# Kernel optimization log

Measured on AMD Instinct MI355X. Metric: run time of the kernel, lower is better.

Reference implementation:

```python
import jax, jax.numpy as jnp
import numpy as np

B = 16384
MV = 512   # movie_vector_size
UV = 512   # user_vector_size
NM = 16    # num_dense_movie_embeddings
NU = 16    # num_dense_user_embeddings
DS = 16    # dense_embedding_size
MLP = [256, 128, 1]


def setup_inputs() -> dict:
    key = jax.random.key(0)
    ks = jax.random.split(key, 12)
    inp = {
        'movie_vectors': jax.random.normal(ks[0], (B, MV), jnp.float32),
        'user_vectors': jax.random.normal(ks[1], (B, UV), jnp.float32),
        # embedding towers: Linear(in, DS*N + 1), stored as [in, out]
        'Wm': jax.random.normal(ks[2], (MV, DS * NM + 1), jnp.float32) * (1.0 / np.sqrt(MV)),
        'bm': jax.random.normal(ks[3], (DS * NM + 1,), jnp.float32) * 0.01,
        'Wu': jax.random.normal(ks[4], (UV, DS * NU + 1), jnp.float32) * (1.0 / np.sqrt(UV)),
        'bu': jax.random.normal(ks[5], (DS * NU + 1,), jnp.float32) * 0.01,
    }
    d_in = (NM + NU) * DS  # 512
    dims = [d_in] + MLP
    for i in range(len(MLP)):
        inp[f'W{i+1}'] = jax.random.normal(ks[6 + 2*i], (dims[i], dims[i+1]), jnp.float32) * (1.0 / np.sqrt(dims[i]))
        inp[f'b{i+1}'] = jax.random.normal(ks[7 + 2*i], (dims[i+1],), jnp.float32) * 0.01
    return inp


def reference(movie_vectors, user_vectors, Wm, bm, Wu, bu, W1, b1, W2, b2, W3, b3):
    batch = movie_vectors.shape[0]
    movie_dense = movie_vectors @ Wm + bm          # [B, DS*NM+1]
    user_dense = user_vectors @ Wu + bu            # [B, DS*NU+1]
    fm_additive = movie_dense[:, -1] + user_dense[:, -1]            # [B]
    m_split = movie_dense[:, :-1].reshape(batch, NM, DS)            # [B, NM, DS]
    u_split = user_dense[:, :-1].reshape(batch, NU, DS)             # [B, NU, DS]
    fm_interactions = jnp.einsum('bik,bjk->bij', m_split, u_split).reshape(batch, -1)  # [B, NM*NU]
    all_dense = jnp.concatenate([movie_dense[:, :-1], user_dense[:, :-1]], axis=-1)    # [B, (NM+NU)*DS]
    h = jax.nn.relu(all_dense @ W1 + b1)
    h = jax.nn.relu(h @ W2 + b2)
    mlp_out = h @ W3 + b3                                           # [B, 1]
    logit = mlp_out + fm_additive[:, None] + jnp.sum(fm_interactions, axis=-1, keepdims=True)
    return logit
```

## Files before the change

kernel.cpp:

```cpp
#include <hip/hip_runtime.h>


#define NTH 512
#define RB  32

typedef __bf16 bf16x8 __attribute__((ext_vector_type(8)));
typedef float  f32x4  __attribute__((ext_vector_type(4)));

#define WS_WMF  0
#define WS_WUF  294912
#define WS_W1F  589824
#define WS_W2F  851968
#define WS_BIAS 917504

#define BPITCH  528
#define L_BST   0
#define L_DENSE 33792
#define L_FM    66560
#define L_ADD   70912
#define L_OUT   71168
#define LDSB    71296

__device__ __forceinline__ unsigned short f2bf(float f) {
  unsigned u = __builtin_bit_cast(unsigned, f);
  u += 0x7FFFu + ((u >> 16) & 1u);
  return (unsigned short)(u >> 16);
}

__device__ __forceinline__ f32x4 mfma_bf16(bf16x8 a, bf16x8 b, f32x4 c) {
  return __builtin_amdgcn_mfma_f32_16x16x32_bf16(a, b, c, 0, 0, 0);
}

extern "C" __global__ __launch_bounds__(256) void deepfm_prep(
    const float* __restrict__ Wm, const float* __restrict__ bm,
    const float* __restrict__ Wu, const float* __restrict__ bu,
    const float* __restrict__ W1, const float* __restrict__ W2,
    const float* __restrict__ b3, char* __restrict__ ws) {
  const int unit = blockIdx.x * 4 + (threadIdx.x >> 6);
  if (unit >= 897) return;
  const int l = threadIdx.x & 63;
  const int fi = l & 15, q = l >> 4;
  unsigned short h[8];
  if (unit < 576) {
    const int t = unit / 288, rem = unit % 288;
    const int kg = rem / 18, ft = rem % 18;
    const float* W = t ? Wu : Wm;
    char* outp = ws + (t ? WS_WUF : WS_WMF);
    const int f = ft * 16 + fi;
#pragma unroll
    for (int e = 0; e < 8; ++e) {
      const int k = kg * 32 + q * 8 + e;
      float val;
      if (f < 256) val = W[k * 257 + f];
      else if (f < 272) {
        float s = 0.f;
#pragma unroll
        for (int i = 0; i < 16; ++i) s += W[k * 257 + i * 16 + (f - 256)];
        val = s;
      } else if (f == 272) val = W[k * 257 + 256];
      else val = 0.f;
      h[e] = f2bf(val);
    }
    uint4 o;
    o.x = h[0] | ((unsigned)h[1] << 16); o.y = h[2] | ((unsigned)h[3] << 16);
    o.z = h[4] | ((unsigned)h[5] << 16); o.w = h[6] | ((unsigned)h[7] << 16);
    *(uint4*)(outp + (((kg * 18 + ft) * 64 + l) << 4)) = o;
  } else if (unit < 832) {
    const int bb = unit - 576;
    const int kg = bb / 16, ft = bb % 16;
    const int f = ft * 16 + fi;
#pragma unroll
    for (int e = 0; e < 8; ++e) h[e] = f2bf(W1[(kg * 32 + q * 8 + e) * 256 + f]);
    uint4 o;
    o.x = h[0] | ((unsigned)h[1] << 16); o.y = h[2] | ((unsigned)h[3] << 16);
    o.z = h[4] | ((unsigned)h[5] << 16); o.w = h[6] | ((unsigned)h[7] << 16);
    *(uint4*)(ws + WS_W1F + (((kg * 16 + ft) * 64 + l) << 4)) = o;
  } else if (unit < 896) {
    const int bb = unit - 832;
    const int kg = bb / 8, ft = bb % 8;
    const int f = ft * 16 + fi;
#pragma unroll
    for (int e = 0; e < 8; ++e) h[e] = f2bf(W2[(kg * 32 + q * 8 + e) * 128 + f]);
    uint4 o;
    o.x = h[0] | ((unsigned)h[1] << 16); o.y = h[2] | ((unsigned)h[3] << 16);
    o.z = h[4] | ((unsigned)h[5] << 16); o.w = h[6] | ((unsigned)h[7] << 16);
    *(uint4*)(ws + WS_W2F + (((kg * 8 + ft) * 64 + l) << 4)) = o;
  } else {
    float* aux = (float*)(ws + WS_BIAS);
    if (l < 16) {
      float s = 0.f;
      for (int i = 0; i < 16; ++i) s += bm[i * 16 + l];
      aux[l] = s;
    } else if (l < 32) {
      const int k = l - 16;
      float s = 0.f;
      for (int i = 0; i < 16; ++i) s += bu[i * 16 + k];
      aux[l] = s;
    } else if (l == 32) {
      aux[32] = bm[256] + bu[256] + b3[0];
    }
  }
}

extern "C" __global__ __launch_bounds__(NTH, 4) void deepfm_main(
    const float* __restrict__ movie, const float* __restrict__ user,
    const float* __restrict__ bm, const float* __restrict__ bu,
    const float* __restrict__ b1, const float* __restrict__ b2,
    const float* __restrict__ W3, const char* __restrict__ ws,
    float* __restrict__ out) {
  extern __shared__ __align__(16) char lds[];
  char* const bstage    = lds + L_BST;
  char* const densefrag = lds + L_DENSE;
  char* const h1frag    = lds + L_BST;
  float* const fmbuf    = (float*)(lds + L_FM);
  float* const addbuf   = (float*)(lds + L_ADD);
  float* const outpart  = (float*)(lds + L_OUT);

  const int tid = threadIdx.x;
  const int w   = tid >> 6;
  const int l   = tid & 63;
  const int cn  = l & 15;
  const int q   = l >> 4;
  const int row0 = blockIdx.x * RB;

  const int tw   = w >> 2;
  const int wi   = w & 3;
  const int axi  = wi & 1;
  const int axrt = wi >> 1;

  const f32x4 zz = {0.f, 0.f, 0.f, 0.f};
  const float* auxb = (const float*)(ws + WS_BIAS);

  {
    const char* WF = ws + (tw ? WS_WUF : WS_WMF);
    const char* brow = bstage + tw * 32 * BPITCH;
    f32x4 a0r0 = zz, a0r1 = zz, a1r0 = zz, a1r1 = zz;
    f32x4 a2r0 = zz, a2r1 = zz, a3r0 = zz, a3r1 = zz;
    f32x4 axc = zz;

    for (int h = 0; h < 2; ++h) {
      if (h) __syncthreads();
#pragma unroll
      for (int p = 0; p < 8; ++p) {
        const int idx = p * 512 + tid;
        const int r = idx >> 6, f4 = idx & 63;
        const float* src = (r >= 32) ? user : movie;
        const float4 v = *(const float4*)(src + (size_t)(row0 + (r & 31)) * 512 +
                                          h * 256 + f4 * 4);
        uint2 o;
        o.x = f2bf(v.x) | ((unsigned)f2bf(v.y) << 16);
        o.y = f2bf(v.z) | ((unsigned)f2bf(v.w) << 16);
        *(uint2*)(bstage + r * BPITCH + f4 * 8) = o;
      }
      __syncthreads();

#pragma unroll 2
      for (int kgl = 0; kgl < 8; ++kgl) {
        const int kg = h * 8 + kgl;
        const bf16x8 bf0 = *(const bf16x8*)(brow + cn * BPITCH + kgl * 64 + q * 16);
        const bf16x8 bf1 = *(const bf16x8*)(brow + (16 + cn) * BPITCH + kgl * 64 + q * 16);
        const bf16x8 A0 = *(const bf16x8*)(WF + (((kg * 18 + wi * 4 + 0) * 64 + l) << 4));
        const bf16x8 A1 = *(const bf16x8*)(WF + (((kg * 18 + wi * 4 + 1) * 64 + l) << 4));
        const bf16x8 A2 = *(const bf16x8*)(WF + (((kg * 18 + wi * 4 + 2) * 64 + l) << 4));
        const bf16x8 A3 = *(const bf16x8*)(WF + (((kg * 18 + wi * 4 + 3) * 64 + l) << 4));
        const bf16x8 AX = *(const bf16x8*)(WF + (((kg * 18 + 16 + axi) * 64 + l) << 4));
        a0r0 = mfma_bf16(A0, bf0, a0r0);  a0r1 = mfma_bf16(A0, bf1, a0r1);
        a1r0 = mfma_bf16(A1, bf0, a1r0);  a1r1 = mfma_bf16(A1, bf1, a1r1);
        a2r0 = mfma_bf16(A2, bf0, a2r0);  a2r1 = mfma_bf16(A2, bf1, a2r1);
        a3r0 = mfma_bf16(A3, bf0, a3r0);  a3r1 = mfma_bf16(A3, bf1, a3r1);
        axc  = mfma_bf16(AX, axrt ? bf1 : bf0, axc);
      }
    }

    const float* bt = tw ? bu : bm;
    const f32x4 accA[4][2] = {{a0r0, a0r1}, {a1r0, a1r1}, {a2r0, a2r1}, {a3r0, a3r1}};
#pragma unroll
    for (int s = 0; s < 4; ++s) {
      const int ft = wi * 4 + s;
      const int fb = ft * 16 + q * 4;
      const float g0 = bt[fb], g1 = bt[fb + 1], g2 = bt[fb + 2], g3 = bt[fb + 3];
      const int kd = tw * 256 + fb;
      const int kgd = kd >> 5, qd = (kd >> 3) & 3, ed = kd & 4;
#pragma unroll
      for (int rt = 0; rt < 2; ++rt) {
        const f32x4 v = accA[s][rt];
        uint2 p;
        p.x = f2bf(v[0] + g0) | ((unsigned)f2bf(v[1] + g1) << 16);
        p.y = f2bf(v[2] + g2) | ((unsigned)f2bf(v[3] + g3) << 16);
        *(uint2*)(densefrag + (((kgd * 2 + rt) * 64 + qd * 16 + cn) << 4) +
                  (ed ? 8 : 0)) = p;
      }
    }

    if (axi == 0) {
#pragma unroll
      for (int reg = 0; reg < 4; ++reg)
        fmbuf[(tw * 32 + axrt * 16 + cn) * 17 + (q * 4 + reg)] = axc[reg];
    } else if (q == 0) {
      addbuf[tw * 32 + axrt * 16 + cn] = axc[0];
    }
  }

  __syncthreads();

  if (tid < 32) {
    float p = 0.f;
#pragma unroll
    for (int k = 0; k < 16; ++k)
      p += (fmbuf[tid * 17 + k] + auxb[k]) *
           (fmbuf[(32 + tid) * 17 + k] + auxb[16 + k]);
    outpart[tid] = p + addbuf[tid] + addbuf[32 + tid] + auxb[32];
  }

  {
    const char* W1F = ws + WS_W1F;
    f32x4 a00 = zz, a01 = zz, a10 = zz, a11 = zz;
#pragma unroll 4
    for (int kg = 0; kg < 16; ++kg) {
      const bf16x8 b0  = *(const bf16x8*)(densefrag + (((kg * 2 + 0) * 64 + l) << 4));
      const bf16x8 b1f = *(const bf16x8*)(densefrag + (((kg * 2 + 1) * 64 + l) << 4));
      const bf16x8 a0 = *(const bf16x8*)(W1F + (((kg * 16 + w) * 64 + l) << 4));
      const bf16x8 a1 = *(const bf16x8*)(W1F + (((kg * 16 + w + 8) * 64 + l) << 4));
      a00 = mfma_bf16(a0, b0,  a00);
      a01 = mfma_bf16(a0, b1f, a01);
      a10 = mfma_bf16(a1, b0,  a10);
      a11 = mfma_bf16(a1, b1f, a11);
    }
    const f32x4 accA[2][2] = {{a00, a01}, {a10, a11}};
#pragma unroll
    for (int s = 0; s < 2; ++s) {
      const int ft = w + s * 8;
      const int fb = ft * 16 + q * 4;
      const float g0 = b1[fb], g1 = b1[fb + 1], g2 = b1[fb + 2], g3 = b1[fb + 3];
      const int kgd = fb >> 5, qd = (fb >> 3) & 3, ed = fb & 4;
#pragma unroll
      for (int rt = 0; rt < 2; ++rt) {
        const f32x4 v = accA[s][rt];
        uint2 p;
        p.x = f2bf(fmaxf(v[0] + g0, 0.f)) | ((unsigned)f2bf(fmaxf(v[1] + g1, 0.f)) << 16);
        p.y = f2bf(fmaxf(v[2] + g2, 0.f)) | ((unsigned)f2bf(fmaxf(v[3] + g3, 0.f)) << 16);
        *(uint2*)(h1frag + (((kgd * 2 + rt) * 64 + qd * 16 + cn) << 4) +
                  (ed ? 8 : 0)) = p;
      }
    }
  }

  __syncthreads();

  {
    const char* W2F = ws + WS_W2F;
    f32x4 d0 = zz, d1 = zz;
#pragma unroll 4
    for (int kg = 0; kg < 8; ++kg) {
      const bf16x8 b0  = *(const bf16x8*)(h1frag + (((kg * 2 + 0) * 64 + l) << 4));
      const bf16x8 b1f = *(const bf16x8*)(h1frag + (((kg * 2 + 1) * 64 + l) << 4));
      const bf16x8 a0 = *(const bf16x8*)(W2F + (((kg * 8 + w) * 64 + l) << 4));
      d0 = mfma_bf16(a0, b0,  d0);
      d1 = mfma_bf16(a0, b1f, d1);
    }
    const int fb = w * 16 + q * 4;
    float bb[4], ww[4];
#pragma unroll
    for (int i = 0; i < 4; ++i) { bb[i] = b2[fb + i]; ww[i] = W3[fb + i]; }
    const f32x4 acc3[2] = {d0, d1};
#pragma unroll
    for (int rt = 0; rt < 2; ++rt) {
      float p = 0.f;
#pragma unroll
      for (int reg = 0; reg < 4; ++reg)
        p += fmaxf(acc3[rt][reg] + bb[reg], 0.f) * ww[reg];
      p += __shfl_xor(p, 16, 64);
      p += __shfl_xor(p, 32, 64);
      if (l < 16) atomicAdd(&outpart[rt * 16 + cn], p);
    }
  }

  __syncthreads();
  if (tid < 32) out[row0 + tid] = outpart[tid];
}

extern "C" void kernel_launch(void* const* d_in, const int* in_sizes, int n_in,
                              void* d_out, int out_size, void* d_ws, size_t ws_size,
                              hipStream_t stream) {
  const float* movie = (const float*)d_in[0];
  const float* user  = (const float*)d_in[1];
  const float* Wm = (const float*)d_in[2];
  const float* bm = (const float*)d_in[3];
  const float* Wu = (const float*)d_in[4];
  const float* bu = (const float*)d_in[5];
  const float* W1 = (const float*)d_in[6];
  const float* b1 = (const float*)d_in[7];
  const float* W2 = (const float*)d_in[8];
  const float* b2 = (const float*)d_in[9];
  const float* W3 = (const float*)d_in[10];
  const float* b3 = (const float*)d_in[11];
  char* ws = (char*)d_ws;
  float* out = (float*)d_out;

  (void)hipFuncSetAttribute((const void*)deepfm_main,
                            hipFuncAttributeMaxDynamicSharedMemorySize, LDSB);

  deepfm_prep<<<225, 256, 0, stream>>>(Wm, bm, Wu, bu, W1, W2, b3, ws);
  deepfm_main<<<512, NTH, LDSB, stream>>>(movie, user, bm, bu, b1, b2, W3, ws, out);
}
```

Baseline: 136.4 us.

## Double rows per block to 64 with 1024 threads, remapping wave work

Each block now handles 64 batch rows with 16 waves instead of 32 rows with 8 waves. Waves are remapped so that each weight fragment loaded from global memory feeds four row tiles instead of two. This halves the number of global weight-fragment loads per row in the embedding tower and W1 stages, and the launch drops to 256 blocks. In exchange LDS use roughly doubles to about 142 KB per block, so at most one block fits per CU, and 256 blocks may underfill a 256-CU MI355X and limit latency hiding.

```diff
diff --git a/kernel.cpp b/kernel.cpp
--- a/kernel.cpp
+++ b/kernel.cpp
@@ -1,8 +1,8 @@
 #include <hip/hip_runtime.h>
 
 
-#define NTH 512
-#define RB  32
+#define NTH 1024
+#define RB  64
 
 typedef __bf16 bf16x8 __attribute__((ext_vector_type(8)));
 typedef float  f32x4  __attribute__((ext_vector_type(4)));
@@ -15,11 +15,11 @@
 
 #define BPITCH  528
 #define L_BST   0
-#define L_DENSE 33792
-#define L_FM    66560
-#define L_ADD   70912
-#define L_OUT   71168
-#define LDSB    71296
+#define L_DENSE 67584
+#define L_FM    133120
+#define L_ADD   141824
+#define L_OUT   142336
+#define LDSB    142592
 
 __device__ __forceinline__ unsigned short f2bf(float f) {
   unsigned u = __builtin_bit_cast(unsigned, f);
@@ -123,8 +123,8 @@
   const int q   = l >> 4;
   const int row0 = blockIdx.x * RB;
 
-  const int tw   = w >> 2;
-  const int wi   = w & 3;
+  const int tw   = w >> 3;
+  const int wi   = w & 7;
   const int axi  = wi & 1;
   const int axrt = wi >> 1;
 
@@ -133,19 +133,19 @@
 
   {
     const char* WF = ws + (tw ? WS_WUF : WS_WMF);
-    const char* brow = bstage + tw * 32 * BPITCH;
-    f32x4 a0r0 = zz, a0r1 = zz, a1r0 = zz, a1r1 = zz;
-    f32x4 a2r0 = zz, a2r1 = zz, a3r0 = zz, a3r1 = zz;
+    const char* brow = bstage + tw * 64 * BPITCH;
+    f32x4 a0r0 = zz, a0r1 = zz, a0r2 = zz, a0r3 = zz;
+    f32x4 a1r0 = zz, a1r1 = zz, a1r2 = zz, a1r3 = zz;
     f32x4 axc = zz;
 
     for (int h = 0; h < 2; ++h) {
       if (h) __syncthreads();
 #pragma unroll
       for (int p = 0; p < 8; ++p) {
-        const int idx = p * 512 + tid;
+        const int idx = p * 1024 + tid;
         const int r = idx >> 6, f4 = idx & 63;
-        const float* src = (r >= 32) ? user : movie;
-        const float4 v = *(const float4*)(src + (size_t)(row0 + (r & 31)) * 512 +
+        const float* src = (r >= 64) ? user : movie;
+        const float4 v = *(const float4*)(src + (size_t)(row0 + (r & 63)) * 512 +
                                           h * 256 + f4 * 4);
         uint2 o;
         o.x = f2bf(v.x) | ((unsigned)f2bf(v.y) << 16);
@@ -159,35 +159,37 @@
         const int kg = h * 8 + kgl;
         const bf16x8 bf0 = *(const bf16x8*)(brow + cn * BPITCH + kgl * 64 + q * 16);
         const bf16x8 bf1 = *(const bf16x8*)(brow + (16 + cn) * BPITCH + kgl * 64 + q * 16);
-        const bf16x8 A0 = *(const bf16x8*)(WF + (((kg * 18 + wi * 4 + 0) * 64 + l) << 4));
-        const bf16x8 A1 = *(const bf16x8*)(WF + (((kg * 18 + wi * 4 + 1) * 64 + l) << 4));
-        const bf16x8 A2 = *(const bf16x8*)(WF + (((kg * 18 + wi * 4 + 2) * 64 + l) << 4));
-        const bf16x8 A3 = *(const bf16x8*)(WF + (((kg * 18 + wi * 4 + 3) * 64 + l) << 4));
+        const bf16x8 bf2 = *(const bf16x8*)(brow + (32 + cn) * BPITCH + kgl * 64 + q * 16);
+        const bf16x8 bf3 = *(const bf16x8*)(brow + (48 + cn) * BPITCH + kgl * 64 + q * 16);
+        const bf16x8 A0 = *(const bf16x8*)(WF + (((kg * 18 + wi * 2 + 0) * 64 + l) << 4));
+        const bf16x8 A1 = *(const bf16x8*)(WF + (((kg * 18 + wi * 2 + 1) * 64 + l) << 4));
         const bf16x8 AX = *(const bf16x8*)(WF + (((kg * 18 + 16 + axi) * 64 + l) << 4));
         a0r0 = mfma_bf16(A0, bf0, a0r0);  a0r1 = mfma_bf16(A0, bf1, a0r1);
+        a0r2 = mfma_bf16(A0, bf2, a0r2);  a0r3 = mfma_bf16(A0, bf3, a0r3);
         a1r0 = mfma_bf16(A1, bf0, a1r0);  a1r1 = mfma_bf16(A1, bf1, a1r1);
-        a2r0 = mfma_bf16(A2, bf0, a2r0);  a2r1 = mfma_bf16(A2, bf1, a2r1);
-        a3r0 = mfma_bf16(A3, bf0, a3r0);  a3r1 = mfma_bf16(A3, bf1, a3r1);
-        axc  = mfma_bf16(AX, axrt ? bf1 : bf0, axc);
+        a1r2 = mfma_bf16(A1, bf2, a1r2);  a1r3 = mfma_bf16(A1, bf3, a1r3);
+        const bf16x8 bsel = (axrt == 0) ? bf0 : (axrt == 1) ? bf1
+                          : (axrt == 2) ? bf2 : bf3;
+        axc = mfma_bf16(AX, bsel, axc);
       }
     }
 
     const float* bt = tw ? bu : bm;
-    const f32x4 accA[4][2] = {{a0r0, a0r1}, {a1r0, a1r1}, {a2r0, a2r1}, {a3r0, a3r1}};
-#pragma unroll
-    for (int s = 0; s < 4; ++s) {
-      const int ft = wi * 4 + s;
+    const f32x4 accA[2][4] = {{a0r0, a0r1, a0r2, a0r3}, {a1r0, a1r1, a1r2, a1r3}};
+#pragma unroll
+    for (int s = 0; s < 2; ++s) {
+      const int ft = wi * 2 + s;
       const int fb = ft * 16 + q * 4;
       const float g0 = bt[fb], g1 = bt[fb + 1], g2 = bt[fb + 2], g3 = bt[fb + 3];
       const int kd = tw * 256 + fb;
       const int kgd = kd >> 5, qd = (kd >> 3) & 3, ed = kd & 4;
 #pragma unroll
-      for (int rt = 0; rt < 2; ++rt) {
+      for (int rt = 0; rt < 4; ++rt) {
         const f32x4 v = accA[s][rt];
         uint2 p;
         p.x = f2bf(v[0] + g0) | ((unsigned)f2bf(v[1] + g1) << 16);
         p.y = f2bf(v[2] + g2) | ((unsigned)f2bf(v[3] + g3) << 16);
-        *(uint2*)(densefrag + (((kgd * 2 + rt) * 64 + qd * 16 + cn) << 4) +
+        *(uint2*)(densefrag + (((kgd * 4 + rt) * 64 + qd * 16 + cn) << 4) +
                   (ed ? 8 : 0)) = p;
       }
     }
@@ -195,53 +197,50 @@
     if (axi == 0) {
 #pragma unroll
       for (int reg = 0; reg < 4; ++reg)
-        fmbuf[(tw * 32 + axrt * 16 + cn) * 17 + (q * 4 + reg)] = axc[reg];
+        fmbuf[(tw * 64 + axrt * 16 + cn) * 17 + (q * 4 + reg)] = axc[reg];
     } else if (q == 0) {
-      addbuf[tw * 32 + axrt * 16 + cn] = axc[0];
+      addbuf[tw * 64 + axrt * 16 + cn] = axc[0];
     }
   }
 
   __syncthreads();
 
-  if (tid < 32) {
+  if (tid < 64) {
     float p = 0.f;
 #pragma unroll
     for (int k = 0; k < 16; ++k)
       p += (fmbuf[tid * 17 + k] + auxb[k]) *
-           (fmbuf[(32 + tid) * 17 + k] + auxb[16 + k]);
-    outpart[tid] = p + addbuf[tid] + addbuf[32 + tid] + auxb[32];
+           (fmbuf[(64 + tid) * 17 + k] + auxb[16 + k]);
+    outpart[tid] = p + addbuf[tid] + addbuf[64 + tid] + auxb[32];
   }
 
   {
     const char* W1F = ws + WS_W1F;
-    f32x4 a00 = zz, a01 = zz, a10 = zz, a11 = zz;
+    f32x4 r0 = zz, r1 = zz, r2 = zz, r3 = zz;
 #pragma unroll 4
     for (int kg = 0; kg < 16; ++kg) {
-      const bf16x8 b0  = *(const bf16x8*)(densefrag + (((kg * 2 + 0) * 64 + l) << 4));
-      const bf16x8 b1f = *(const bf16x8*)(densefrag + (((kg * 2 + 1) * 64 + l) << 4));
+      const bf16x8 b0 = *(const bf16x8*)(densefrag + (((kg * 4 + 0) * 64 + l) << 4));
+      const bf16x8 b1f = *(const bf16x8*)(densefrag + (((kg * 4 + 1) * 64 + l) << 4));
+      const bf16x8 b2f = *(const bf16x8*)(densefrag + (((kg * 4 + 2) * 64 + l) << 4));
+      const bf16x8 b3f = *(const bf16x8*)(densefrag + (((kg * 4 + 3) * 64 + l) << 4));
       const bf16x8 a0 = *(const bf16x8*)(W1F + (((kg * 16 + w) * 64 + l) << 4));
-      const bf16x8 a1 = *(const bf16x8*)(W1F + (((kg * 16 + w + 8) * 64 + l) << 4));
-      a00 = mfma_bf16(a0, b0,  a00);
-      a01 = mfma_bf16(a0, b1f, a01);
-      a10 = mfma_bf16(a1, b0,  a10);
-      a11 = mfma_bf16(a1, b1f, a11);
-    }
-    const f32x4 accA[2][2] = {{a00, a01}, {a10, a11}};
-#pragma unroll
-    for (int s = 0; s < 2; ++s) {
-      const int ft = w + s * 8;
-      const int fb = ft * 16 + q * 4;
-      const float g0 = b1[fb], g1 = b1[fb + 1], g2 = b1[fb + 2], g3 = b1[fb + 3];
-      const int kgd = fb >> 5, qd = (fb >> 3) & 3, ed = fb & 4;
-#pragma unroll
-      for (int rt = 0; rt < 2; ++rt) {
-        const f32x4 v = accA[s][rt];
-        uint2 p;
-        p.x = f2bf(fmaxf(v[0] + g0, 0.f)) | ((unsigned)f2bf(fmaxf(v[1] + g1, 0.f)) << 16);
-        p.y = f2bf(fmaxf(v[2] + g2, 0.f)) | ((unsigned)f2bf(fmaxf(v[3] + g3, 0.f)) << 16);
-        *(uint2*)(h1frag + (((kgd * 2 + rt) * 64 + qd * 16 + cn) << 4) +
-                  (ed ? 8 : 0)) = p;
-      }
+      r0 = mfma_bf16(a0, b0,  r0);
+      r1 = mfma_bf16(a0, b1f, r1);
+      r2 = mfma_bf16(a0, b2f, r2);
+      r3 = mfma_bf16(a0, b3f, r3);
+    }
+    const f32x4 accA[4] = {r0, r1, r2, r3};
+    const int fb = w * 16 + q * 4;
+    const float g0 = b1[fb], g1 = b1[fb + 1], g2 = b1[fb + 2], g3 = b1[fb + 3];
+    const int kgd = fb >> 5, qd = (fb >> 3) & 3, ed = fb & 4;
+#pragma unroll
+    for (int rt = 0; rt < 4; ++rt) {
+      const f32x4 v = accA[rt];
+      uint2 p;
+      p.x = f2bf(fmaxf(v[0] + g0, 0.f)) | ((unsigned)f2bf(fmaxf(v[1] + g1, 0.f)) << 16);
+      p.y = f2bf(fmaxf(v[2] + g2, 0.f)) | ((unsigned)f2bf(fmaxf(v[3] + g3, 0.f)) << 16);
+      *(uint2*)(h1frag + (((kgd * 4 + rt) * 64 + qd * 16 + cn) << 4) +
+                (ed ? 8 : 0)) = p;
     }
   }
 
@@ -249,26 +248,29 @@
 
   {
     const char* W2F = ws + WS_W2F;
+    const int ftw = w & 7;
+    const int rth = w >> 3;
     f32x4 d0 = zz, d1 = zz;
 #pragma unroll 4
     for (int kg = 0; kg < 8; ++kg) {
-      const bf16x8 b0  = *(const bf16x8*)(h1frag + (((kg * 2 + 0) * 64 + l) << 4));
-      const bf16x8 b1f = *(const bf16x8*)(h1frag + (((kg * 2 + 1) * 64 + l) << 4));
-      const bf16x8 a0 = *(const bf16x8*)(W2F + (((kg * 8 + w) * 64 + l) << 4));
+      const bf16x8 b0 = *(const bf16x8*)(h1frag + (((kg * 4 + rth * 2 + 0) * 64 + l) << 4));
+      const bf16x8 b1f = *(const bf16x8*)(h1frag + (((kg * 4 + rth * 2 + 1) * 64 + l) << 4));
+      const bf16x8 a0 = *(const bf16x8*)(W2F + (((kg * 8 + ftw) * 64 + l) << 4));
       d0 = mfma_bf16(a0, b0,  d0);
       d1 = mfma_bf16(a0, b1f, d1);
     }
-    const int fb = w * 16 + q * 4;
+    const int fb = ftw * 16 + q * 4;
     float bb[4], ww[4];
 #pragma unroll
     for (int i = 0; i < 4; ++i) { bb[i] = b2[fb + i]; ww[i] = W3[fb + i]; }
     const f32x4 acc3[2] = {d0, d1};
 #pragma unroll
-    for (int rt = 0; rt < 2; ++rt) {
+    for (int j = 0; j < 2; ++j) {
+      const int rt = rth * 2 + j;
       float p = 0.f;
 #pragma unroll
       for (int reg = 0; reg < 4; ++reg)
-        p += fmaxf(acc3[rt][reg] + bb[reg], 0.f) * ww[reg];
+        p += fmaxf(acc3[j][reg] + bb[reg], 0.f) * ww[reg];
       p += __shfl_xor(p, 16, 64);
       p += __shfl_xor(p, 32, 64);
       if (l < 16) atomicAdd(&outpart[rt * 16 + cn], p);
@@ -276,7 +278,7 @@
   }
 
   __syncthreads();
-  if (tid < 32) out[row0 + tid] = outpart[tid];
+  if (tid < 64) out[row0 + tid] = outpart[tid];
 }
 
 extern "C" void kernel_launch(void* const* d_in, const int* in_sizes, int n_in,
@@ -301,5 +303,5 @@
                             hipFuncAttributeMaxDynamicSharedMemorySize, LDSB);
 
   deepfm_prep<<<225, 256, 0, stream>>>(Wm, bm, Wu, bu, W1, W2, b3, ws);
-  deepfm_main<<<512, NTH, LDSB, stream>>>(movie, user, bm, bu, b1, b2, W3, ws, out);
-}
+  deepfm_main<<<256, NTH, LDSB, stream>>>(movie, user, bm, bu, b1, b2, W3, ws, out);
+}
```

Result: faster. 131.7 us, median of 2 (-3.4%).
